# Optimization experiments

Measured on AMD Instinct MI355X. Metric: run time of the kernel, lower is better.

## Reference

```python
import jax, jax.numpy as jnp
import numpy as np
from jax import lax

N_LAYERS = 30
KERNEL = 5
MU = 255.0  # quantization_channels=256 -> mu = 255
DILATIONS = [(2 ** k) % 10 for k in range(N_LAYERS)]  # 2^k mod (n_layers/n_cycles)


def causal_conv1d(x, w, b, dilation):
    # x: [B,1,T], w: [1,1,K], b: [1]; left-pad so output is causal, same length.
    pad = (w.shape[-1] - 1) * dilation
    xp = jnp.pad(x, ((0, 0), (0, 0), (pad, 0)))
    y = lax.conv_general_dilated(xp, w, window_strides=(1,), padding='VALID',
                                 rhs_dilation=(dilation,),
                                 dimension_numbers=('NCH', 'OIH', 'NCH'))
    return y + b[None, :, None]


def setup_inputs() -> dict:
    key = jax.random.key(0)
    ks = jax.random.split(key, 12)
    B, T = 8, 262144
    s = 0.2  # keep gated activations away from saturation
    return {
        'x': jax.random.normal(ks[0], (B, 1, T), dtype=jnp.float32),
        'causal_w': jax.random.normal(ks[1], (1, 1, KERNEL), jnp.float32) * s,
        'causal_b': jnp.zeros((1,), jnp.float32),
        'filter_w': jax.random.normal(ks[2], (N_LAYERS, 1, 1, KERNEL), jnp.float32) * s,
        'filter_b': jax.random.normal(ks[3], (N_LAYERS, 1), jnp.float32) * s,
        'gate_w': jax.random.normal(ks[4], (N_LAYERS, 1, 1, KERNEL), jnp.float32) * s,
        'gate_b': jax.random.normal(ks[5], (N_LAYERS, 1), jnp.float32) * s,
        'res_w': jax.random.normal(ks[6], (N_LAYERS, 1, 1, 1), jnp.float32) * s,
        'res_b': jax.random.normal(ks[7], (N_LAYERS, 1), jnp.float32) * s,
        'conv1_w': jax.random.normal(ks[8], (1, 1, 1), jnp.float32) * s,
        'conv1_b': jnp.zeros((1,), jnp.float32),
        'conv2_w': jax.random.normal(ks[9], (1, 1, 1), jnp.float32) * s,
        'conv2_b': jnp.zeros((1,), jnp.float32),
    }


def reference(x, causal_w, causal_b, filter_w, filter_b, gate_w, gate_b,
              res_w, res_b, conv1_w, conv1_b, conv2_w, conv2_b):
    h = causal_conv1d(x, causal_w, causal_b, 1)
    skip_sum = jnp.zeros_like(h)
    for k in range(N_LAYERS):  # fixed small layer loop; dilation is static per layer
        d = DILATIONS[k]
        f = jnp.tanh(causal_conv1d(h, filter_w[k], filter_b[k], d))
        g = jax.nn.sigmoid(causal_conv1d(h, gate_w[k], gate_b[k], d))
        z = f * g
        skip_sum = skip_sum + z
        # 1x1 residual conv (1 channel) = scale + bias, then residual add
        h = z * res_w[k][0, 0, 0] + res_b[k][0] + h
    out = jax.nn.relu(skip_sum) * conv1_w[0, 0, 0] + conv1_b[0]
    out = jax.nn.relu(out) * conv2_w[0, 0, 0] + conv2_b[0]
    # mu-law expanding
    out = jnp.sign(out) * (jnp.power(1.0 + MU, jnp.abs(out)) - 1.0) / MU
    return jax.nn.softmax(out, axis=-1)
```

## Files before the change

### kernel.cpp

```cpp
#include <hip/hip_runtime.h>
#include <cmath>

#define T_LEN 262144
#define NROW 8
#define NL 30
#define NT 512
#define PPT 3
#define EXT (NT * PPT * 2)
#define HALO 576
#define TILE (EXT - HALO)
#define PB ((T_LEN + TILE - 1) / TILE)
#define PAD 32
#define CH 4096
#define RB (T_LEN / CH)
#define NB2 (NROW * RB)

#define NEG2LOG2E -2.885390082f
#define NEGLOG2E  -1.4426950409f

#if __has_builtin(__builtin_amdgcn_exp2f)
#define EXP2(x) __builtin_amdgcn_exp2f(x)
#else
#define EXP2(x) __expf(0.6931471805599453f * (x))
#endif

typedef float f32x2 __attribute__((ext_vector_type(2)));

__device__ __forceinline__ float fast_rcp(float x) { return __builtin_amdgcn_rcpf(x); }

__device__ __forceinline__ f32x2 exp2v(f32x2 x) {
    f32x2 r; r.x = EXP2(x.x); r.y = EXP2(x.y); return r;
}
__device__ __forceinline__ f32x2 rcpv(f32x2 x) {
    f32x2 r; r.x = fast_rcp(x.x); r.y = fast_rcp(x.y); return r;
}

template<int D, int CUT, bool WB>
__device__ __forceinline__ void layerv(
    int k,
    const float* __restrict__ fw, const float* __restrict__ fb,
    const float* __restrict__ gw, const float* __restrict__ gb,
    const float* __restrict__ rw, const float* __restrict__ rb,
    const float* __restrict__ src, float* __restrict__ dst,
    f32x2 (&h)[PPT], f32x2 (&skip)[PPT], int tid)
{
    const float f0 = fw[k*5+0], f1 = fw[k*5+1], f2 = fw[k*5+2], f3 = fw[k*5+3], f4 = fw[k*5+4];
    const float fbk = fb[k];
    const float g0 = gw[k*5+0], g1 = gw[k*5+1], g2 = gw[k*5+2], g3 = gw[k*5+3], g4 = gw[k*5+4];
    const float gbk = gb[k];
    const float rwk = rw[k], rbk = rb[k];

    #pragma unroll
    for (int p = 0; p < PPT; ++p) {
        const int i2 = 2 * (tid + p * NT);
        if (2 * p * NT < CUT) {
            if ((i2 + 1) < CUT) continue;
        }

        const f32x2 v0 = *(const f32x2*)&src[i2 - 4*D];
        const f32x2 v1 = *(const f32x2*)&src[i2 - 3*D];
        const f32x2 v2 = *(const f32x2*)&src[i2 - 2*D];
        const f32x2 v3 = *(const f32x2*)&src[i2 -   D];
        const f32x2 v4 = h[p];

        f32x2 af = fbk + f0 * v0;
        af = f1 * v1 + af;
        af = f2 * v2 + af;
        af = f3 * v3 + af;
        af = f4 * v4 + af;
        f32x2 ag = gbk + g0 * v0;
        ag = g1 * v1 + ag;
        ag = g2 * v2 + ag;
        ag = g3 * v3 + ag;
        ag = g4 * v4 + ag;

        const f32x2 u = exp2v(af * NEG2LOG2E);
        const f32x2 w = exp2v(ag * NEGLOG2E);
        const f32x2 num = 1.0f - u;
        const f32x2 den = (1.0f + u) * (1.0f + w);
        const f32x2 z = num * rcpv(den);
        skip[p] += z;
        if (WB) {
            h[p] = (z * rwk + rbk) + v4;
            *(f32x2*)&dst[i2] = h[p];
        }
    }
    if (WB) __syncthreads();
}

__device__ __forceinline__ void layer_d1(
    const float* __restrict__ fw, const float* __restrict__ fb,
    const float* __restrict__ gw, const float* __restrict__ gb,
    const float* __restrict__ rw, const float* __restrict__ rb,
    const float* __restrict__ src, float* __restrict__ dst,
    f32x2 (&h)[PPT], f32x2 (&skip)[PPT], int tid)
{
    const float f0 = fw[0], f1 = fw[1], f2 = fw[2], f3 = fw[3], f4 = fw[4];
    const float fbk = fb[0];
    const float g0 = gw[0], g1 = gw[1], g2 = gw[2], g3 = gw[3], g4 = gw[4];
    const float gbk = gb[0];
    const float rwk = rw[0], rbk = rb[0];

    #pragma unroll
    for (int p = 0; p < PPT; ++p) {
        const int i2 = 2 * (tid + p * NT);
        const f32x2 a = *(const f32x2*)&src[i2 - 4];
        const f32x2 b = *(const f32x2*)&src[i2 - 2];
        const f32x2 c = h[p];
        f32x2 v0, v1, v2, v3;
        v0.x = a.x; v0.y = a.y;
        v1.x = a.y; v1.y = b.x;
        v2.x = b.x; v2.y = b.y;
        v3.x = b.y; v3.y = c.x;

        f32x2 af = fbk + f0 * v0;
        af = f1 * v1 + af;
        af = f2 * v2 + af;
        af = f3 * v3 + af;
        af = f4 * c  + af;
        f32x2 ag = gbk + g0 * v0;
        ag = g1 * v1 + ag;
        ag = g2 * v2 + ag;
        ag = g3 * v3 + ag;
        ag = g4 * c  + ag;

        const f32x2 u = exp2v(af * NEG2LOG2E);
        const f32x2 w = exp2v(ag * NEGLOG2E);
        const f32x2 num = 1.0f - u;
        const f32x2 den = (1.0f + u) * (1.0f + w);
        const f32x2 z = num * rcpv(den);
        skip[p] += z;
        h[p] = (z * rwk + rbk) + c;
        *(f32x2*)&dst[i2] = h[p];
    }
    __syncthreads();
}

__global__ __launch_bounds__(NT, 8)
void k_wavenet(const float* __restrict__ x,
               const float* __restrict__ cw,  const float* __restrict__ cb,
               const float* __restrict__ fw,  const float* __restrict__ fb,
               const float* __restrict__ gw,  const float* __restrict__ gb,
               const float* __restrict__ rw,  const float* __restrict__ rb,
               const float* __restrict__ c1w, const float* __restrict__ c1b,
               const float* __restrict__ c2w, const float* __restrict__ c2b,
               float* __restrict__ eout, float* __restrict__ partsum)
{
    __shared__ __align__(16) float hrawA[PAD + EXT];
    __shared__ __align__(16) float hrawB[PAD + EXT];
    __shared__ float reds[NT / 64];
    float* bufA = hrawA + PAD;
    float* bufB = hrawB + PAD;

    const int tid  = threadIdx.x;
    const int row  = blockIdx.x / PB;
    const int tile = blockIdx.x % PB;
    const int t0   = tile * TILE;

    if (tid < PAD) { hrawA[tid] = 0.0f; hrawB[tid] = 0.0f; }

    const float* xr = x + (size_t)row * T_LEN;
    f32x2 h[PPT], skip[PPT];
    #pragma unroll
    for (int p = 0; p < PPT; ++p) {
        const int i2 = 2 * (tid + p * NT);
        const int g = t0 - HALO + i2;
        f32x2 v;
        v.x = (g     >= 0 && g     < T_LEN) ? xr[g]     : 0.0f;
        v.y = (g + 1 >= 0 && g + 1 < T_LEN) ? xr[g + 1] : 0.0f;
        *(f32x2*)&bufA[i2] = v;
        h[p] = v;
        skip[p].x = 0.0f; skip[p].y = 0.0f;
    }
    __syncthreads();

    {
        const float w0 = cw[0], w1 = cw[1], w2 = cw[2], w3 = cw[3], w4 = cw[4];
        const float b  = cb[0];
        #pragma unroll
        for (int p = 0; p < PPT; ++p) {
            const int i2 = 2 * (tid + p * NT);
            const f32x2 a  = *(const f32x2*)&bufA[i2 - 4];
            const f32x2 bb = *(const f32x2*)&bufA[i2 - 2];
            const f32x2 c  = h[p];
            f32x2 v0, v1, v2, v3;
            v0.x = a.x;  v0.y = a.y;
            v1.x = a.y;  v1.y = bb.x;
            v2.x = bb.x; v2.y = bb.y;
            v3.x = bb.y; v3.y = c.x;
            f32x2 acc = b + w0 * v0;
            acc = w1 * v1 + acc;
            acc = w2 * v2 + acc;
            acc = w3 * v3 + acc;
            acc = w4 * c  + acc;
            h[p] = acc;
            *(f32x2*)&bufB[i2] = acc;
        }
        __syncthreads();
    }

    layer_d1(fw, fb, gw, gb, rw, rb, bufB, bufA, h, skip, tid);
    layerv<2,  16, true >( 1, fw, fb, gw, gb, rw, rb, bufA, bufB, h, skip, tid);
    layerv<4,  32, true >( 2, fw, fb, gw, gb, rw, rb, bufB, bufA, h, skip, tid);
    layerv<8,  64, true >( 3, fw, fb, gw, gb, rw, rb, bufA, bufB, h, skip, tid);
    layerv<6,  88, true >( 4, fw, fb, gw, gb, rw, rb, bufB, bufA, h, skip, tid);
    layerv<2,  96, true >( 5, fw, fb, gw, gb, rw, rb, bufA, bufB, h, skip, tid);
    layerv<4, 112, true >( 6, fw, fb, gw, gb, rw, rb, bufB, bufA, h, skip, tid);
    layerv<8, 144, true >( 7, fw, fb, gw, gb, rw, rb, bufA, bufB, h, skip, tid);
    layerv<6, 168, true >( 8, fw, fb, gw, gb, rw, rb, bufB, bufA, h, skip, tid);
    layerv<2, 176, true >( 9, fw, fb, gw, gb, rw, rb, bufA, bufB, h, skip, tid);
    layerv<4, 192, true >(10, fw, fb, gw, gb, rw, rb, bufB, bufA, h, skip, tid);
    layerv<8, 224, true >(11, fw, fb, gw, gb, rw, rb, bufA, bufB, h, skip, tid);
    layerv<6, 248, true >(12, fw, fb, gw, gb, rw, rb, bufB, bufA, h, skip, tid);
    layerv<2, 256, true >(13, fw, fb, gw, gb, rw, rb, bufA, bufB, h, skip, tid);
    layerv<4, 272, true >(14, fw, fb, gw, gb, rw, rb, bufB, bufA, h, skip, tid);
    layerv<8, 304, true >(15, fw, fb, gw, gb, rw, rb, bufA, bufB, h, skip, tid);
    layerv<6, 328, true >(16, fw, fb, gw, gb, rw, rb, bufB, bufA, h, skip, tid);
    layerv<2, 336, true >(17, fw, fb, gw, gb, rw, rb, bufA, bufB, h, skip, tid);
    layerv<4, 352, true >(18, fw, fb, gw, gb, rw, rb, bufB, bufA, h, skip, tid);
    layerv<8, 384, true >(19, fw, fb, gw, gb, rw, rb, bufA, bufB, h, skip, tid);
    layerv<6, 408, true >(20, fw, fb, gw, gb, rw, rb, bufB, bufA, h, skip, tid);
    layerv<2, 416, true >(21, fw, fb, gw, gb, rw, rb, bufA, bufB, h, skip, tid);
    layerv<4, 432, true >(22, fw, fb, gw, gb, rw, rb, bufB, bufA, h, skip, tid);
    layerv<8, 464, true >(23, fw, fb, gw, gb, rw, rb, bufA, bufB, h, skip, tid);
    layerv<6, 488, true >(24, fw, fb, gw, gb, rw, rb, bufB, bufA, h, skip, tid);
    layerv<2, 496, true >(25, fw, fb, gw, gb, rw, rb, bufA, bufB, h, skip, tid);
    layerv<4, 512, true >(26, fw, fb, gw, gb, rw, rb, bufB, bufA, h, skip, tid);
    layerv<8, 544, true >(27, fw, fb, gw, gb, rw, rb, bufA, bufB, h, skip, tid);
    layerv<6, 568, true >(28, fw, fb, gw, gb, rw, rb, bufB, bufA, h, skip, tid);
    layerv<2, 576, false>(29, fw, fb, gw, gb, rw, rb, bufA, bufB, h, skip, tid);

    const float w1 = c1w[0], b1 = c1b[0], w2 = c2w[0], b2 = c2b[0];
    float s = 0.0f;
    float* er = eout + (size_t)row * T_LEN;
    #pragma unroll
    for (int p = 0; p < PPT; ++p) {
        const int i2 = 2 * (tid + p * NT);
        if (i2 >= HALO) {
            const int t = t0 + i2 - HALO;
            if (t < T_LEN) {
                f32x2 sk = skip[p];
                float ox = fmaf(fmaxf(sk.x, 0.0f), w1, b1);
                float oy = fmaf(fmaxf(sk.y, 0.0f), w1, b1);
                ox = fmaf(fmaxf(ox, 0.0f), w2, b2);
                oy = fmaf(fmaxf(oy, 0.0f), w2, b2);
                float vx = fmaf(EXP2(8.0f * fabsf(ox)), (1.0f/255.0f), -(1.0f/255.0f));
                float vy = fmaf(EXP2(8.0f * fabsf(oy)), (1.0f/255.0f), -(1.0f/255.0f));
                vx = copysignf(vx, ox);
                vy = copysignf(vy, oy);
                const float ex = __expf(vx);
                const float ey = __expf(vy);
                f32x2 e; e.x = ex; e.y = ey;
                *(f32x2*)&er[t] = e;
                s += ex + ey;
            }
        }
    }
    #pragma unroll
    for (int off = 32; off >= 1; off >>= 1) s += __shfl_xor(s, off, 64);
    if ((tid & 63) == 0) reds[tid >> 6] = s;
    __syncthreads();
    if (tid == 0) {
        float ss = 0.0f;
        #pragma unroll
        for (int w = 0; w < NT / 64; ++w) ss += reds[w];
        partsum[blockIdx.x] = ss;
    }
}

__global__ __launch_bounds__(256)
void k_scale(float* __restrict__ ebuf, const float* __restrict__ partsum)
{
    const int tid = threadIdx.x;
    const int row = blockIdx.x / RB;

    __shared__ float red[4];
    float s = 0.0f;
    for (int j = tid; j < PB; j += 256) s += partsum[row * PB + j];
    #pragma unroll
    for (int off = 32; off >= 1; off >>= 1) s += __shfl_xor(s, off, 64);
    if ((tid & 63) == 0) red[tid >> 6] = s;
    __syncthreads();
    const float tot = (red[0] + red[1]) + (red[2] + red[3]);
    const float inv = 1.0f / tot;

    float4* vp = (float4*)(ebuf + (size_t)blockIdx.x * CH);
    #pragma unroll
    for (int q = 0; q < 4; ++q) {
        float4 v = vp[tid + q * 256];
        v.x *= inv; v.y *= inv; v.z *= inv; v.w *= inv;
        vp[tid + q * 256] = v;
    }
}

extern "C" void kernel_launch(void* const* d_in, const int* in_sizes, int n_in,
                              void* d_out, int out_size, void* d_ws, size_t ws_size,
                              hipStream_t stream)
{
    const float* x   = (const float*)d_in[0];
    const float* cw  = (const float*)d_in[1];
    const float* cb  = (const float*)d_in[2];
    const float* fw  = (const float*)d_in[3];
    const float* fb  = (const float*)d_in[4];
    const float* gw  = (const float*)d_in[5];
    const float* gb  = (const float*)d_in[6];
    const float* rw  = (const float*)d_in[7];
    const float* rb  = (const float*)d_in[8];
    const float* c1w = (const float*)d_in[9];
    const float* c1b = (const float*)d_in[10];
    const float* c2w = (const float*)d_in[11];
    const float* c2b = (const float*)d_in[12];

    float* eout    = (float*)d_out;
    float* partsum = (float*)d_ws;

    k_wavenet<<<NROW * PB, NT, 0, stream>>>(x, cw, cb, fw, fb, gw, gb, rw, rb,
                                            c1w, c1b, c2w, c2b, eout, partsum);
    k_scale<<<NB2, 256, 0, stream>>>(eout, partsum);
}
```

Before: 144.3 us.

## Process two time tiles per block interleaved to share barriers and add ILP

Each block now carries two independent tiles through all 30 gated layers, with separate double-buffered LDS arrays for each. One __syncthreads per layer then serves both tiles, and the two independent dependency chains give the scheduler more instruction-level parallelism. This halves the grid, raises LDS per block and register pressure, and relaxes the launch-bounds occupancy hint. The softmax scale kernel is adjusted to read one partial sum per paired block and to use smaller chunks, which gives it more blocks.

```diff
diff --git a/kernel.cpp b/kernel.cpp
--- a/kernel.cpp
+++ b/kernel.cpp
@@ -9,9 +9,10 @@
 #define EXT (NT * PPT * 2)
 #define HALO 576
 #define TILE (EXT - HALO)
-#define PB ((T_LEN + TILE - 1) / TILE)
+#define PB 106
+#define JB (PB / 2)
 #define PAD 32
-#define CH 4096
+#define CH 2048
 #define RB (T_LEN / CH)
 #define NB2 (NROW * RB)
 
@@ -36,13 +37,15 @@
 }
 
 template<int D, int CUT, bool WB>
-__device__ __forceinline__ void layerv(
+__device__ __forceinline__ void layer2(
     int k,
     const float* __restrict__ fw, const float* __restrict__ fb,
     const float* __restrict__ gw, const float* __restrict__ gb,
     const float* __restrict__ rw, const float* __restrict__ rb,
-    const float* __restrict__ src, float* __restrict__ dst,
-    f32x2 (&h)[PPT], f32x2 (&skip)[PPT], int tid)
+    const float* __restrict__ s0, float* __restrict__ d0,
+    const float* __restrict__ s1, float* __restrict__ d1,
+    f32x2 (&h0)[PPT], f32x2 (&sk0)[PPT],
+    f32x2 (&h1)[PPT], f32x2 (&sk1)[PPT], int tid)
 {
     const float f0 = fw[k*5+0], f1 = fw[k*5+1], f2 = fw[k*5+2], f3 = fw[k*5+3], f4 = fw[k*5+4];
     const float fbk = fb[k];
@@ -50,50 +53,56 @@
     const float gbk = gb[k];
     const float rwk = rw[k], rbk = rb[k];
 
-    #pragma unroll
-    for (int p = 0; p < PPT; ++p) {
-        const int i2 = 2 * (tid + p * NT);
-        if (2 * p * NT < CUT) {
-            if ((i2 + 1) < CUT) continue;
+    auto body = [&](const float* __restrict__ src, float* __restrict__ dst,
+                    f32x2 (&h)[PPT], f32x2 (&skip)[PPT]) {
+        #pragma unroll
+        for (int p = 0; p < PPT; ++p) {
+            const int i2 = 2 * (tid + p * NT);
+            if (2 * p * NT < CUT) {
+                if ((i2 + 1) < CUT) continue;
+            }
+            const f32x2 v0 = *(const f32x2*)&src[i2 - 4*D];
+            const f32x2 v1 = *(const f32x2*)&src[i2 - 3*D];
+            const f32x2 v2 = *(const f32x2*)&src[i2 - 2*D];
+            const f32x2 v3 = *(const f32x2*)&src[i2 -   D];
+            const f32x2 v4 = h[p];
+
+            f32x2 af = fbk + f0 * v0;
+            af = f1 * v1 + af;
+            af = f2 * v2 + af;
+            af = f3 * v3 + af;
+            af = f4 * v4 + af;
+            f32x2 ag = gbk + g0 * v0;
+            ag = g1 * v1 + ag;
+            ag = g2 * v2 + ag;
+            ag = g3 * v3 + ag;
+            ag = g4 * v4 + ag;
+
+            const f32x2 u = exp2v(af * NEG2LOG2E);
+            const f32x2 w = exp2v(ag * NEGLOG2E);
+            const f32x2 num = 1.0f - u;
+            const f32x2 den = (1.0f + u) * (1.0f + w);
+            const f32x2 z = num * rcpv(den);
+            skip[p] += z;
+            if (WB) {
+                h[p] = (z * rwk + rbk) + v4;
+                *(f32x2*)&dst[i2] = h[p];
+            }
         }
-
-        const f32x2 v0 = *(const f32x2*)&src[i2 - 4*D];
-        const f32x2 v1 = *(const f32x2*)&src[i2 - 3*D];
-        const f32x2 v2 = *(const f32x2*)&src[i2 - 2*D];
-        const f32x2 v3 = *(const f32x2*)&src[i2 -   D];
-        const f32x2 v4 = h[p];
-
-        f32x2 af = fbk + f0 * v0;
-        af = f1 * v1 + af;
-        af = f2 * v2 + af;
-        af = f3 * v3 + af;
-        af = f4 * v4 + af;
-        f32x2 ag = gbk + g0 * v0;
-        ag = g1 * v1 + ag;
-        ag = g2 * v2 + ag;
-        ag = g3 * v3 + ag;
-        ag = g4 * v4 + ag;
-
-        const f32x2 u = exp2v(af * NEG2LOG2E);
-        const f32x2 w = exp2v(ag * NEGLOG2E);
-        const f32x2 num = 1.0f - u;
-        const f32x2 den = (1.0f + u) * (1.0f + w);
-        const f32x2 z = num * rcpv(den);
-        skip[p] += z;
-        if (WB) {
-            h[p] = (z * rwk + rbk) + v4;
-            *(f32x2*)&dst[i2] = h[p];
-        }
-    }
+    };
+    body(s0, d0, h0, sk0);
+    body(s1, d1, h1, sk1);
     if (WB) __syncthreads();
 }
 
-__device__ __forceinline__ void layer_d1(
+__device__ __forceinline__ void layer2_d1(
     const float* __restrict__ fw, const float* __restrict__ fb,
     const float* __restrict__ gw, const float* __restrict__ gb,
     const float* __restrict__ rw, const float* __restrict__ rb,
-    const float* __restrict__ src, float* __restrict__ dst,
-    f32x2 (&h)[PPT], f32x2 (&skip)[PPT], int tid)
+    const float* __restrict__ s0, float* __restrict__ d0,
+    const float* __restrict__ s1, float* __restrict__ d1,
+    f32x2 (&h0)[PPT], f32x2 (&sk0)[PPT],
+    f32x2 (&h1)[PPT], f32x2 (&sk1)[PPT], int tid)
 {
     const float f0 = fw[0], f1 = fw[1], f2 = fw[2], f3 = fw[3], f4 = fw[4];
     const float fbk = fb[0];
@@ -101,42 +110,47 @@
     const float gbk = gb[0];
     const float rwk = rw[0], rbk = rb[0];
 
-    #pragma unroll
-    for (int p = 0; p < PPT; ++p) {
-        const int i2 = 2 * (tid + p * NT);
-        const f32x2 a = *(const f32x2*)&src[i2 - 4];
-        const f32x2 b = *(const f32x2*)&src[i2 - 2];
-        const f32x2 c = h[p];
-        f32x2 v0, v1, v2, v3;
-        v0.x = a.x; v0.y = a.y;
-        v1.x = a.y; v1.y = b.x;
-        v2.x = b.x; v2.y = b.y;
-        v3.x = b.y; v3.y = c.x;
-
-        f32x2 af = fbk + f0 * v0;
-        af = f1 * v1 + af;
-        af = f2 * v2 + af;
-        af = f3 * v3 + af;
-        af = f4 * c  + af;
-        f32x2 ag = gbk + g0 * v0;
-        ag = g1 * v1 + ag;
-        ag = g2 * v2 + ag;
-        ag = g3 * v3 + ag;
-        ag = g4 * c  + ag;
-
-        const f32x2 u = exp2v(af * NEG2LOG2E);
-        const f32x2 w = exp2v(ag * NEGLOG2E);
-        const f32x2 num = 1.0f - u;
-        const f32x2 den = (1.0f + u) * (1.0f + w);
-        const f32x2 z = num * rcpv(den);
-        skip[p] += z;
-        h[p] = (z * rwk + rbk) + c;
-        *(f32x2*)&dst[i2] = h[p];
-    }
+    auto body = [&](const float* __restrict__ src, float* __restrict__ dst,
+                    f32x2 (&h)[PPT], f32x2 (&skip)[PPT]) {
+        #pragma unroll
+        for (int p = 0; p < PPT; ++p) {
+            const int i2 = 2 * (tid + p * NT);
+            const f32x2 a = *(const f32x2*)&src[i2 - 4];
+            const f32x2 b = *(const f32x2*)&src[i2 - 2];
+            const f32x2 c = h[p];
+            f32x2 v0, v1, v2, v3;
+            v0.x = a.x; v0.y = a.y;
+            v1.x = a.y; v1.y = b.x;
+            v2.x = b.x; v2.y = b.y;
+            v3.x = b.y; v3.y = c.x;
+
+            f32x2 af = fbk + f0 * v0;
+            af = f1 * v1 + af;
+            af = f2 * v2 + af;
+            af = f3 * v3 + af;
+            af = f4 * c  + af;
+            f32x2 ag = gbk + g0 * v0;
+            ag = g1 * v1 + ag;
+            ag = g2 * v2 + ag;
+            ag = g3 * v3 + ag;
+            ag = g4 * c  + ag;
+
+            const f32x2 u = exp2v(af * NEG2LOG2E);
+            const f32x2 w = exp2v(ag * NEGLOG2E);
+            const f32x2 num = 1.0f - u;
+            const f32x2 den = (1.0f + u) * (1.0f + w);
+            const f32x2 z = num * rcpv(den);
+            skip[p] += z;
+            h[p] = (z * rwk + rbk) + c;
+            *(f32x2*)&dst[i2] = h[p];
+        }
+    };
+    body(s0, d0, h0, sk0);
+    body(s1, d1, h1, sk1);
     __syncthreads();
 }
 
-__global__ __launch_bounds__(NT, 8)
+__global__ __launch_bounds__(NT, 4)
 void k_wavenet(const float* __restrict__ x,
                const float* __restrict__ cw,  const float* __restrict__ cb,
                const float* __restrict__ fw,  const float* __restrict__ fb,
@@ -146,116 +160,135 @@
                const float* __restrict__ c2w, const float* __restrict__ c2b,
                float* __restrict__ eout, float* __restrict__ partsum)
 {
-    __shared__ __align__(16) float hrawA[PAD + EXT];
-    __shared__ __align__(16) float hrawB[PAD + EXT];
+    __shared__ __align__(16) float rA0[PAD + EXT];
+    __shared__ __align__(16) float rB0[PAD + EXT];
+    __shared__ __align__(16) float rA1[PAD + EXT];
+    __shared__ __align__(16) float rB1[PAD + EXT];
     __shared__ float reds[NT / 64];
-    float* bufA = hrawA + PAD;
-    float* bufB = hrawB + PAD;
-
-    const int tid  = threadIdx.x;
-    const int row  = blockIdx.x / PB;
-    const int tile = blockIdx.x % PB;
-    const int t0   = tile * TILE;
-
-    if (tid < PAD) { hrawA[tid] = 0.0f; hrawB[tid] = 0.0f; }
+    float* A0 = rA0 + PAD;  float* B0 = rB0 + PAD;
+    float* A1 = rA1 + PAD;  float* B1 = rB1 + PAD;
+
+    const int tid = threadIdx.x;
+    const int row = blockIdx.x / JB;
+    const int jj  = blockIdx.x % JB;
+    const int t0a = (2 * jj)     * TILE;
+    const int t0b = (2 * jj + 1) * TILE;
+
+    if (tid < PAD) { rA0[tid] = 0.0f; rB0[tid] = 0.0f; rA1[tid] = 0.0f; rB1[tid] = 0.0f; }
 
     const float* xr = x + (size_t)row * T_LEN;
-    f32x2 h[PPT], skip[PPT];
-    #pragma unroll
-    for (int p = 0; p < PPT; ++p) {
-        const int i2 = 2 * (tid + p * NT);
-        const int g = t0 - HALO + i2;
-        f32x2 v;
-        v.x = (g     >= 0 && g     < T_LEN) ? xr[g]     : 0.0f;
-        v.y = (g + 1 >= 0 && g + 1 < T_LEN) ? xr[g + 1] : 0.0f;
-        *(f32x2*)&bufA[i2] = v;
-        h[p] = v;
-        skip[p].x = 0.0f; skip[p].y = 0.0f;
+    f32x2 h0[PPT], sk0[PPT], h1[PPT], sk1[PPT];
+
+    {
+        auto stage = [&](int t0, float* buf, f32x2 (&h)[PPT], f32x2 (&skip)[PPT]) {
+            #pragma unroll
+            for (int p = 0; p < PPT; ++p) {
+                const int i2 = 2 * (tid + p * NT);
+                const int g = t0 - HALO + i2;
+                f32x2 v;
+                v.x = (g     >= 0 && g     < T_LEN) ? xr[g]     : 0.0f;
+                v.y = (g + 1 >= 0 && g + 1 < T_LEN) ? xr[g + 1] : 0.0f;
+                *(f32x2*)&buf[i2] = v;
+                h[p] = v;
+                skip[p].x = 0.0f; skip[p].y = 0.0f;
+            }
+        };
+        stage(t0a, A0, h0, sk0);
+        stage(t0b, A1, h1, sk1);
+        __syncthreads();
     }
-    __syncthreads();
 
     {
         const float w0 = cw[0], w1 = cw[1], w2 = cw[2], w3 = cw[3], w4 = cw[4];
         const float b  = cb[0];
+        auto iconv = [&](const float* src, float* dst, f32x2 (&h)[PPT]) {
+            #pragma unroll
+            for (int p = 0; p < PPT; ++p) {
+                const int i2 = 2 * (tid + p * NT);
+                const f32x2 a  = *(const f32x2*)&src[i2 - 4];
+                const f32x2 bb = *(const f32x2*)&src[i2 - 2];
+                const f32x2 c  = h[p];
+                f32x2 v0, v1, v2, v3;
+                v0.x = a.x;  v0.y = a.y;
+                v1.x = a.y;  v1.y = bb.x;
+                v2.x = bb.x; v2.y = bb.y;
+                v3.x = bb.y; v3.y = c.x;
+                f32x2 acc = b + w0 * v0;
+                acc = w1 * v1 + acc;
+                acc = w2 * v2 + acc;
+                acc = w3 * v3 + acc;
+                acc = w4 * c  + acc;
+                h[p] = acc;
+                *(f32x2*)&dst[i2] = acc;
+            }
+        };
+        iconv(A0, B0, h0);
+        iconv(A1, B1, h1);
+        __syncthreads();
+    }
+
+    layer2_d1(fw, fb, gw, gb, rw, rb, B0, A0, B1, A1, h0, sk0, h1, sk1, tid);
+    layer2<2,  16, true >( 1, fw, fb, gw, gb, rw, rb, A0, B0, A1, B1, h0, sk0, h1, sk1, tid);
+    layer2<4,  32, true >( 2, fw, fb, gw, gb, rw, rb, B0, A0, B1, A1, h0, sk0, h1, sk1, tid);
+    layer2<8,  64, true >( 3, fw, fb, gw, gb, rw, rb, A0, B0, A1, B1, h0, sk0, h1, sk1, tid);
+    layer2<6,  88, true >( 4, fw, fb, gw, gb, rw, rb, B0, A0, B1, A1, h0, sk0, h1, sk1, tid);
+    layer2<2,  96, true >( 5, fw, fb, gw, gb, rw, rb, A0, B0, A1, B1, h0, sk0, h1, sk1, tid);
+    layer2<4, 112, true >( 6, fw, fb, gw, gb, rw, rb, B0, A0, B1, A1, h0, sk0, h1, sk1, tid);
+    layer2<8, 144, true >( 7, fw, fb, gw, gb, rw, rb, A0, B0, A1, B1, h0, sk0, h1, sk1, tid);
+    layer2<6, 168, true >( 8, fw, fb, gw, gb, rw, rb, B0, A0, B1, A1, h0, sk0, h1, sk1, tid);
+    layer2<2, 176, true >( 9, fw, fb, gw, gb, rw, rb, A0, B0, A1, B1, h0, sk0, h1, sk1, tid);
+    layer2<4, 192, true >(10, fw, fb, gw, gb, rw, rb, B0, A0, B1, A1, h0, sk0, h1, sk1, tid);
+    layer2<8, 224, true >(11, fw, fb, gw, gb, rw, rb, A0, B0, A1, B1, h0, sk0, h1, sk1, tid);
+    layer2<6, 248, true >(12, fw, fb, gw, gb, rw, rb, B0, A0, B1, A1, h0, sk0, h1, sk1, tid);
+    layer2<2, 256, true >(13, fw, fb, gw, gb, rw, rb, A0, B0, A1, B1, h0, sk0, h1, sk1, tid);
+    layer2<4, 272, true >(14, fw, fb, gw, gb, rw, rb, B0, A0, B1, A1, h0, sk0, h1, sk1, tid);
+    layer2<8, 304, true >(15, fw, fb, gw, gb, rw, rb, A0, B0, A1, B1, h0, sk0, h1, sk1, tid);
+    layer2<6, 328, true >(16, fw, fb, gw, gb, rw, rb, B0, A0, B1, A1, h0, sk0, h1, sk1, tid);
+    layer2<2, 336, true >(17, fw, fb, gw, gb, rw, rb, A0, B0, A1, B1, h0, sk0, h1, sk1, tid);
+    layer2<4, 352, true >(18, fw, fb, gw, gb, rw, rb, B0, A0, B1, A1, h0, sk0, h1, sk1, tid);
+    layer2<8, 384, true >(19, fw, fb, gw, gb, rw, rb, A0, B0, A1, B1, h0, sk0, h1, sk1, tid);
+    layer2<6, 408, true >(20, fw, fb, gw, gb, rw, rb, B0, A0, B1, A1, h0, sk0, h1, sk1, tid);
+    layer2<2, 416, true >(21, fw, fb, gw, gb, rw, rb, A0, B0, A1, B1, h0, sk0, h1, sk1, tid);
+    layer2<4, 432, true >(22, fw, fb, gw, gb, rw, rb, B0, A0, B1, A1, h0, sk0, h1, sk1, tid);
+    layer2<8, 464, true >(23, fw, fb, gw, gb, rw, rb, A0, B0, A1, B1, h0, sk0, h1, sk1, tid);
+    layer2<6, 488, true >(24, fw, fb, gw, gb, rw, rb, B0, A0, B1, A1, h0, sk0, h1, sk1, tid);
+    layer2<2, 496, true >(25, fw, fb, gw, gb, rw, rb, A0, B0, A1, B1, h0, sk0, h1, sk1, tid);
+    layer2<4, 512, true >(26, fw, fb, gw, gb, rw, rb, B0, A0, B1, A1, h0, sk0, h1, sk1, tid);
+    layer2<8, 544, true >(27, fw, fb, gw, gb, rw, rb, A0, B0, A1, B1, h0, sk0, h1, sk1, tid);
+    layer2<6, 568, true >(28, fw, fb, gw, gb, rw, rb, B0, A0, B1, A1, h0, sk0, h1, sk1, tid);
+    layer2<2, 576, false>(29, fw, fb, gw, gb, rw, rb, A0, B0, A1, B1, h0, sk0, h1, sk1, tid);
+
+    const float w1 = c1w[0], b1 = c1b[0], w2 = c2w[0], b2 = c2b[0];
+    float s = 0.0f;
+    float* er = eout + (size_t)row * T_LEN;
+    auto epi = [&](int t0, f32x2 (&skip)[PPT]) {
         #pragma unroll
         for (int p = 0; p < PPT; ++p) {
             const int i2 = 2 * (tid + p * NT);
-            const f32x2 a  = *(const f32x2*)&bufA[i2 - 4];
-            const f32x2 bb = *(const f32x2*)&bufA[i2 - 2];
-            const f32x2 c  = h[p];
-            f32x2 v0, v1, v2, v3;
-            v0.x = a.x;  v0.y = a.y;
-            v1.x = a.y;  v1.y = bb.x;
-            v2.x = bb.x; v2.y = bb.y;
-            v3.x = bb.y; v3.y = c.x;
-            f32x2 acc = b + w0 * v0;
-            acc = w1 * v1 + acc;
-            acc = w2 * v2 + acc;
-            acc = w3 * v3 + acc;
-            acc = w4 * c  + acc;
-            h[p] = acc;
-            *(f32x2*)&bufB[i2] = acc;
+            if (i2 >= HALO) {
+                const int t = t0 + i2 - HALO;
+                if (t < T_LEN) {
+                    f32x2 sk = skip[p];
+                    float ox = fmaf(fmaxf(sk.x, 0.0f), w1, b1);
+                    float oy = fmaf(fmaxf(sk.y, 0.0f), w1, b1);
+                    ox = fmaf(fmaxf(ox, 0.0f), w2, b2);
+                    oy = fmaf(fmaxf(oy, 0.0f), w2, b2);
+                    float vx = fmaf(EXP2(8.0f * fabsf(ox)), (1.0f/255.0f), -(1.0f/255.0f));
+                    float vy = fmaf(EXP2(8.0f * fabsf(oy)), (1.0f/255.0f), -(1.0f/255.0f));
+                    vx = copysignf(vx, ox);
+                    vy = copysignf(vy, oy);
+                    const float ex = __expf(vx);
+                    const float ey = __expf(vy);
+                    f32x2 e; e.x = ex; e.y = ey;
+                    *(f32x2*)&er[t] = e;
+                    s += ex + ey;
+                }
+            }
         }
-        __syncthreads();
-    }
-
-    layer_d1(fw, fb, gw, gb, rw, rb, bufB, bufA, h, skip, tid);
-    layerv<2,  16, true >( 1, fw, fb, gw, gb, rw, rb, bufA, bufB, h, skip, tid);
-    layerv<4,  32, true >( 2, fw, fb, gw, gb, rw, rb, bufB, bufA, h, skip, tid);
-    layerv<8,  64, true >( 3, fw, fb, gw, gb, rw, rb, bufA, bufB, h, skip, tid);
-    layerv<6,  88, true >( 4, fw, fb, gw, gb, rw, rb, bufB, bufA, h, skip, tid);
-    layerv<2,  96, true >( 5, fw, fb, gw, gb, rw, rb, bufA, bufB, h, skip, tid);
-    layerv<4, 112, true >( 6, fw, fb, gw, gb, rw, rb, bufB, bufA, h, skip, tid);
-    layerv<8, 144, true >( 7, fw, fb, gw, gb, rw, rb, bufA, bufB, h, skip, tid);
-    layerv<6, 168, true >( 8, fw, fb, gw, gb, rw, rb, bufB, bufA, h, skip, tid);
-    layerv<2, 176, true >( 9, fw, fb, gw, gb, rw, rb, bufA, bufB, h, skip, tid);
-    layerv<4, 192, true >(10, fw, fb, gw, gb, rw, rb, bufB, bufA, h, skip, tid);
-    layerv<8, 224, true >(11, fw, fb, gw, gb, rw, rb, bufA, bufB, h, skip, tid);
-    layerv<6, 248, true >(12, fw, fb, gw, gb, rw, rb, bufB, bufA, h, skip, tid);
-    layerv<2, 256, true >(13, fw, fb, gw, gb, rw, rb, bufA, bufB, h, skip, tid);
-    layerv<4, 272, true >(14, fw, fb, gw, gb, rw, rb, bufB, bufA, h, skip, tid);
-    layerv<8, 304, true >(15, fw, fb, gw, gb, rw, rb, bufA, bufB, h, skip, tid);
-    layerv<6, 328, true >(16, fw, fb, gw, gb, rw, rb, bufB, bufA, h, skip, tid);
-    layerv<2, 336, true >(17, fw, fb, gw, gb, rw, rb, bufA, bufB, h, skip, tid);
-    layerv<4, 352, true >(18, fw, fb, gw, gb, rw, rb, bufB, bufA, h, skip, tid);
-    layerv<8, 384, true >(19, fw, fb, gw, gb, rw, rb, bufA, bufB, h, skip, tid);
-    layerv<6, 408, true >(20, fw, fb, gw, gb, rw, rb, bufB, bufA, h, skip, tid);
-    layerv<2, 416, true >(21, fw, fb, gw, gb, rw, rb, bufA, bufB, h, skip, tid);
-    layerv<4, 432, true >(22, fw, fb, gw, gb, rw, rb, bufB, bufA, h, skip, tid);
-    layerv<8, 464, true >(23, fw, fb, gw, gb, rw, rb, bufA, bufB, h, skip, tid);
-    layerv<6, 488, true >(24, fw, fb, gw, gb, rw, rb, bufB, bufA, h, skip, tid);
-    layerv<2, 496, true >(25, fw, fb, gw, gb, rw, rb, bufA, bufB, h, skip, tid);
-    layerv<4, 512, true >(26, fw, fb, gw, gb, rw, rb, bufB, bufA, h, skip, tid);
-    layerv<8, 544, true >(27, fw, fb, gw, gb, rw, rb, bufA, bufB, h, skip, tid);
-    layerv<6, 568, true >(28, fw, fb, gw, gb, rw, rb, bufB, bufA, h, skip, tid);
-    layerv<2, 576, false>(29, fw, fb, gw, gb, rw, rb, bufA, bufB, h, skip, tid);
-
-    const float w1 = c1w[0], b1 = c1b[0], w2 = c2w[0], b2 = c2b[0];
-    float s = 0.0f;
-    float* er = eout + (size_t)row * T_LEN;
-    #pragma unroll
-    for (int p = 0; p < PPT; ++p) {
-        const int i2 = 2 * (tid + p * NT);
-        if (i2 >= HALO) {
-            const int t = t0 + i2 - HALO;
-            if (t < T_LEN) {
-                f32x2 sk = skip[p];
-                float ox = fmaf(fmaxf(sk.x, 0.0f), w1, b1);
-                float oy = fmaf(fmaxf(sk.y, 0.0f), w1, b1);
-                ox = fmaf(fmaxf(ox, 0.0f), w2, b2);
-                oy = fmaf(fmaxf(oy, 0.0f), w2, b2);
-                float vx = fmaf(EXP2(8.0f * fabsf(ox)), (1.0f/255.0f), -(1.0f/255.0f));
-                float vy = fmaf(EXP2(8.0f * fabsf(oy)), (1.0f/255.0f), -(1.0f/255.0f));
-                vx = copysignf(vx, ox);
-                vy = copysignf(vy, oy);
-                const float ex = __expf(vx);
-                const float ey = __expf(vy);
-                f32x2 e; e.x = ex; e.y = ey;
-                *(f32x2*)&er[t] = e;
-                s += ex + ey;
-            }
-        }
-    }
+    };
+    epi(t0a, sk0);
+    epi(t0b, sk1);
+
     #pragma unroll
     for (int off = 32; off >= 1; off >>= 1) s += __shfl_xor(s, off, 64);
     if ((tid & 63) == 0) reds[tid >> 6] = s;
@@ -275,8 +308,7 @@
     const int row = blockIdx.x / RB;
 
     __shared__ float red[4];
-    float s = 0.0f;
-    for (int j = tid; j < PB; j += 256) s += partsum[row * PB + j];
+    float s = (tid < JB) ? partsum[row * JB + tid] : 0.0f;
     #pragma unroll
     for (int off = 32; off >= 1; off >>= 1) s += __shfl_xor(s, off, 64);
     if ((tid & 63) == 0) red[tid >> 6] = s;
@@ -286,7 +318,7 @@
 
     float4* vp = (float4*)(ebuf + (size_t)blockIdx.x * CH);
     #pragma unroll
-    for (int q = 0; q < 4; ++q) {
+    for (int q = 0; q < 2; ++q) {
         float4 v = vp[tid + q * 256];
         v.x *= inv; v.y *= inv; v.z *= inv; v.w *= inv;
         vp[tid + q * 256] = v;
@@ -314,7 +346,7 @@
     float* eout    = (float*)d_out;
     float* partsum = (float*)d_ws;
 
-    k_wavenet<<<NROW * PB, NT, 0, stream>>>(x, cw, cb, fw, fb, gw, gb, rw, rb,
+    k_wavenet<<<NROW * JB, NT, 0, stream>>>(x, cw, cb, fw, fb, gw, gb, rw, rb,
                                             c1w, c1b, c2w, c2b, eout, partsum);
     k_scale<<<NB2, 256, 0, stream>>>(eout, partsum);
 }
```

New measurement: 152.8 us. 1.06x slower.

## Give each thread 8 contiguous samples and reuse dilated taps from registers

Applied to the files above, without the earlier changes.

Each thread now owns 8 consecutive time steps instead of 3 strided pairs, with 384 threads per block covering the same 3072-sample tile. Dilated-conv taps that fall inside the thread's own chunk come from registers, and only the halo before the chunk is read from shared memory with 16-byte loads. Global input loads, shared-memory write-backs and output stores are widened to float4. This cuts LDS traffic and instruction count per layer, at the cost of more registers per thread, a lower occupancy hint, and coarser per-thread skipping of halo work.

```diff
diff --git a/kernel.cpp b/kernel.cpp
--- a/kernel.cpp
+++ b/kernel.cpp
@@ -3,13 +3,11 @@
 
 #define T_LEN 262144
 #define NROW 8
-#define NL 30
-#define NT 512
-#define PPT 3
-#define EXT (NT * PPT * 2)
+#define NT 384
+#define EXT 3072
 #define HALO 576
 #define TILE (EXT - HALO)
-#define PB ((T_LEN + TILE - 1) / TILE)
+#define PB 106
 #define PAD 32
 #define CH 4096
 #define RB (T_LEN / CH)
@@ -25,6 +23,7 @@
 #endif
 
 typedef float f32x2 __attribute__((ext_vector_type(2)));
+typedef float f32x4 __attribute__((ext_vector_type(4)));
 
 __device__ __forceinline__ float fast_rcp(float x) { return __builtin_amdgcn_rcpf(x); }
 
@@ -34,15 +33,20 @@
 __device__ __forceinline__ f32x2 rcpv(f32x2 x) {
     f32x2 r; r.x = fast_rcp(x.x); r.y = fast_rcp(x.y); return r;
 }
+__device__ __forceinline__ f32x2 gatedv(f32x2 af, f32x2 ag) {
+    const f32x2 u = exp2v(af * NEG2LOG2E);
+    const f32x2 w = exp2v(ag * NEGLOG2E);
+    return (1.0f - u) * rcpv((1.0f + u) * (1.0f + w));
+}
 
 template<int D, int CUT, bool WB>
-__device__ __forceinline__ void layerv(
+__device__ __forceinline__ void layer8(
     int k,
     const float* __restrict__ fw, const float* __restrict__ fb,
     const float* __restrict__ gw, const float* __restrict__ gb,
     const float* __restrict__ rw, const float* __restrict__ rb,
     const float* __restrict__ src, float* __restrict__ dst,
-    f32x2 (&h)[PPT], f32x2 (&skip)[PPT], int tid)
+    f32x2 (&h)[4], f32x2 (&skip)[4], int base)
 {
     const float f0 = fw[k*5+0], f1 = fw[k*5+1], f2 = fw[k*5+2], f3 = fw[k*5+3], f4 = fw[k*5+4];
     const float fbk = fb[k];
@@ -50,17 +54,76 @@
     const float gbk = gb[k];
     const float rwk = rw[k], rbk = rb[k];
 
+    if (base >= CUT) {
+        f32x2 halo[2*D];
+        #pragma unroll
+        for (int j = 0; j < D; ++j) {
+            const f32x4 t4 = *(const f32x4*)&src[base - 4*D + 4*j];
+            f32x2 lo; lo.x = t4.x; lo.y = t4.y;
+            f32x2 hi; hi.x = t4.z; hi.y = t4.w;
+            halo[2*j]   = lo;
+            halo[2*j+1] = hi;
+        }
+        #pragma unroll
+        for (int p = 3; p >= 0; --p) {
+            const int r4 = p - 4*(D/2);
+            const int r3 = p - 3*(D/2);
+            const int r2 = p - 2*(D/2);
+            const int r1 = p - 1*(D/2);
+            const f32x2 v0 = (r4 >= 0) ? h[r4] : halo[2*D + r4];
+            const f32x2 v1 = (r3 >= 0) ? h[r3] : halo[2*D + r3];
+            const f32x2 v2 = (r2 >= 0) ? h[r2] : halo[2*D + r2];
+            const f32x2 v3 = (r1 >= 0) ? h[r1] : halo[2*D + r1];
+            const f32x2 v4 = h[p];
+
+            f32x2 af = fbk + f0 * v0;
+            af = f1 * v1 + af;
+            af = f2 * v2 + af;
+            af = f3 * v3 + af;
+            af = f4 * v4 + af;
+            f32x2 ag = gbk + g0 * v0;
+            ag = g1 * v1 + ag;
+            ag = g2 * v2 + ag;
+            ag = g3 * v3 + ag;
+            ag = g4 * v4 + ag;
+
+            const f32x2 z = gatedv(af, ag);
+            skip[p] += z;
+            if (WB) h[p] = (z * rwk + rbk) + v4;
+        }
+        if (WB) {
+            f32x4 lo; lo.x = h[0].x; lo.y = h[0].y; lo.z = h[1].x; lo.w = h[1].y;
+            f32x4 hi; hi.x = h[2].x; hi.y = h[2].y; hi.z = h[3].x; hi.w = h[3].y;
+            *(f32x4*)&dst[base]     = lo;
+            *(f32x4*)&dst[base + 4] = hi;
+        }
+    }
+    if (WB) __syncthreads();
+}
+
+__device__ __forceinline__ void layer8_d1(
+    const float* __restrict__ fw, const float* __restrict__ fb,
+    const float* __restrict__ gw, const float* __restrict__ gb,
+    const float* __restrict__ rw, const float* __restrict__ rb,
+    const float* __restrict__ src, float* __restrict__ dst,
+    f32x2 (&h)[4], f32x2 (&skip)[4], int base)
+{
+    const float f0 = fw[0], f1 = fw[1], f2 = fw[2], f3 = fw[3], f4 = fw[4];
+    const float fbk = fb[0];
+    const float g0 = gw[0], g1 = gw[1], g2 = gw[2], g3 = gw[3], g4 = gw[4];
+    const float gbk = gb[0];
+    const float rwk = rw[0], rbk = rb[0];
+
+    const f32x4 hl = *(const f32x4*)&src[base - 4];
+    const float w[12] = {hl.x, hl.y, hl.z, hl.w,
+                         h[0].x, h[0].y, h[1].x, h[1].y,
+                         h[2].x, h[2].y, h[3].x, h[3].y};
     #pragma unroll
-    for (int p = 0; p < PPT; ++p) {
-        const int i2 = 2 * (tid + p * NT);
-        if (2 * p * NT < CUT) {
-            if ((i2 + 1) < CUT) continue;
-        }
-
-        const f32x2 v0 = *(const f32x2*)&src[i2 - 4*D];
-        const f32x2 v1 = *(const f32x2*)&src[i2 - 3*D];
-        const f32x2 v2 = *(const f32x2*)&src[i2 - 2*D];
-        const f32x2 v3 = *(const f32x2*)&src[i2 -   D];
+    for (int p = 0; p < 4; ++p) {
+        f32x2 v0; v0.x = w[2*p+0]; v0.y = w[2*p+1];
+        f32x2 v1; v1.x = w[2*p+1]; v1.y = w[2*p+2];
+        f32x2 v2; v2.x = w[2*p+2]; v2.y = w[2*p+3];
+        f32x2 v3; v3.x = w[2*p+3]; v3.y = w[2*p+4];
         const f32x2 v4 = h[p];
 
         f32x2 af = fbk + f0 * v0;
@@ -74,69 +137,18 @@
         ag = g3 * v3 + ag;
         ag = g4 * v4 + ag;
 
-        const f32x2 u = exp2v(af * NEG2LOG2E);
-        const f32x2 w = exp2v(ag * NEGLOG2E);
-        const f32x2 num = 1.0f - u;
-        const f32x2 den = (1.0f + u) * (1.0f + w);
-        const f32x2 z = num * rcpv(den);
+        const f32x2 z = gatedv(af, ag);
         skip[p] += z;
-        if (WB) {
-            h[p] = (z * rwk + rbk) + v4;
-            *(f32x2*)&dst[i2] = h[p];
-        }
-    }
-    if (WB) __syncthreads();
-}
-
-__device__ __forceinline__ void layer_d1(
-    const float* __restrict__ fw, const float* __restrict__ fb,
-    const float* __restrict__ gw, const float* __restrict__ gb,
-    const float* __restrict__ rw, const float* __restrict__ rb,
-    const float* __restrict__ src, float* __restrict__ dst,
-    f32x2 (&h)[PPT], f32x2 (&skip)[PPT], int tid)
-{
-    const float f0 = fw[0], f1 = fw[1], f2 = fw[2], f3 = fw[3], f4 = fw[4];
-    const float fbk = fb[0];
-    const float g0 = gw[0], g1 = gw[1], g2 = gw[2], g3 = gw[3], g4 = gw[4];
-    const float gbk = gb[0];
-    const float rwk = rw[0], rbk = rb[0];
-
-    #pragma unroll
-    for (int p = 0; p < PPT; ++p) {
-        const int i2 = 2 * (tid + p * NT);
-        const f32x2 a = *(const f32x2*)&src[i2 - 4];
-        const f32x2 b = *(const f32x2*)&src[i2 - 2];
-        const f32x2 c = h[p];
-        f32x2 v0, v1, v2, v3;
-        v0.x = a.x; v0.y = a.y;
-        v1.x = a.y; v1.y = b.x;
-        v2.x = b.x; v2.y = b.y;
-        v3.x = b.y; v3.y = c.x;
-
-        f32x2 af = fbk + f0 * v0;
-        af = f1 * v1 + af;
-        af = f2 * v2 + af;
-        af = f3 * v3 + af;
-        af = f4 * c  + af;
-        f32x2 ag = gbk + g0 * v0;
-        ag = g1 * v1 + ag;
-        ag = g2 * v2 + ag;
-        ag = g3 * v3 + ag;
-        ag = g4 * c  + ag;
-
-        const f32x2 u = exp2v(af * NEG2LOG2E);
-        const f32x2 w = exp2v(ag * NEGLOG2E);
-        const f32x2 num = 1.0f - u;
-        const f32x2 den = (1.0f + u) * (1.0f + w);
-        const f32x2 z = num * rcpv(den);
-        skip[p] += z;
-        h[p] = (z * rwk + rbk) + c;
-        *(f32x2*)&dst[i2] = h[p];
-    }
+        h[p] = (z * rwk + rbk) + v4;
+    }
+    f32x4 lo; lo.x = h[0].x; lo.y = h[0].y; lo.z = h[1].x; lo.w = h[1].y;
+    f32x4 hi; hi.x = h[2].x; hi.y = h[2].y; hi.z = h[3].x; hi.w = h[3].y;
+    *(f32x4*)&dst[base]     = lo;
+    *(f32x4*)&dst[base + 4] = hi;
     __syncthreads();
 }
 
-__global__ __launch_bounds__(NT, 8)
+__global__ __launch_bounds__(NT, 4)
 void k_wavenet(const float* __restrict__ x,
                const float* __restrict__ cw,  const float* __restrict__ cb,
                const float* __restrict__ fw,  const float* __restrict__ fb,
@@ -146,99 +158,123 @@
                const float* __restrict__ c2w, const float* __restrict__ c2b,
                float* __restrict__ eout, float* __restrict__ partsum)
 {
-    __shared__ __align__(16) float hrawA[PAD + EXT];
-    __shared__ __align__(16) float hrawB[PAD + EXT];
+    __shared__ __align__(16) float rA[PAD + EXT];
+    __shared__ __align__(16) float rB[PAD + EXT];
     __shared__ float reds[NT / 64];
-    float* bufA = hrawA + PAD;
-    float* bufB = hrawB + PAD;
+    float* A = rA + PAD;
+    float* B = rB + PAD;
 
     const int tid  = threadIdx.x;
+    const int base = 8 * tid;
     const int row  = blockIdx.x / PB;
     const int tile = blockIdx.x % PB;
     const int t0   = tile * TILE;
 
-    if (tid < PAD) { hrawA[tid] = 0.0f; hrawB[tid] = 0.0f; }
+    if (tid < PAD / 4) {
+        f32x4 z4; z4.x = 0.f; z4.y = 0.f; z4.z = 0.f; z4.w = 0.f;
+        *(f32x4*)&rA[4*tid] = z4;
+        *(f32x4*)&rB[4*tid] = z4;
+    }
 
     const float* xr = x + (size_t)row * T_LEN;
-    f32x2 h[PPT], skip[PPT];
-    #pragma unroll
-    for (int p = 0; p < PPT; ++p) {
-        const int i2 = 2 * (tid + p * NT);
-        const int g = t0 - HALO + i2;
-        f32x2 v;
-        v.x = (g     >= 0 && g     < T_LEN) ? xr[g]     : 0.0f;
-        v.y = (g + 1 >= 0 && g + 1 < T_LEN) ? xr[g + 1] : 0.0f;
-        *(f32x2*)&bufA[i2] = v;
-        h[p] = v;
-        skip[p].x = 0.0f; skip[p].y = 0.0f;
+
+    if (t0 - HALO >= 0 && t0 - HALO + EXT <= T_LEN) {
+        #pragma unroll
+        for (int j = 0; j < 2; ++j) {
+            const int s = tid + j * NT;
+            *(f32x4*)&A[4*s] = *(const f32x4*)&xr[t0 - HALO + 4*s];
+        }
+    } else {
+        #pragma unroll
+        for (int j = 0; j < 2; ++j) {
+            const int s = tid + j * NT;
+            const int g = t0 - HALO + 4*s;
+            f32x4 v;
+            v.x = (g   >= 0 && g   < T_LEN) ? xr[g]   : 0.0f;
+            v.y = (g+1 >= 0 && g+1 < T_LEN) ? xr[g+1] : 0.0f;
+            v.z = (g+2 >= 0 && g+2 < T_LEN) ? xr[g+2] : 0.0f;
+            v.w = (g+3 >= 0 && g+3 < T_LEN) ? xr[g+3] : 0.0f;
+            *(f32x4*)&A[4*s] = v;
+        }
     }
     __syncthreads();
 
+    f32x2 h[4], skip[4];
     {
-        const float w0 = cw[0], w1 = cw[1], w2 = cw[2], w3 = cw[3], w4 = cw[4];
-        const float b  = cb[0];
-        #pragma unroll
-        for (int p = 0; p < PPT; ++p) {
-            const int i2 = 2 * (tid + p * NT);
-            const f32x2 a  = *(const f32x2*)&bufA[i2 - 4];
-            const f32x2 bb = *(const f32x2*)&bufA[i2 - 2];
-            const f32x2 c  = h[p];
-            f32x2 v0, v1, v2, v3;
-            v0.x = a.x;  v0.y = a.y;
-            v1.x = a.y;  v1.y = bb.x;
-            v2.x = bb.x; v2.y = bb.y;
-            v3.x = bb.y; v3.y = c.x;
-            f32x2 acc = b + w0 * v0;
-            acc = w1 * v1 + acc;
-            acc = w2 * v2 + acc;
-            acc = w3 * v3 + acc;
-            acc = w4 * c  + acc;
+        const f32x4 a = *(const f32x4*)&A[base];
+        const f32x4 b = *(const f32x4*)&A[base + 4];
+        h[0].x = a.x; h[0].y = a.y; h[1].x = a.z; h[1].y = a.w;
+        h[2].x = b.x; h[2].y = b.y; h[3].x = b.z; h[3].y = b.w;
+        #pragma unroll
+        for (int p = 0; p < 4; ++p) { skip[p].x = 0.f; skip[p].y = 0.f; }
+    }
+
+    {
+        const float q0 = cw[0], q1 = cw[1], q2 = cw[2], q3 = cw[3], q4 = cw[4];
+        const float qb = cb[0];
+        const f32x4 hl = *(const f32x4*)&A[base - 4];
+        const float w[12] = {hl.x, hl.y, hl.z, hl.w,
+                             h[0].x, h[0].y, h[1].x, h[1].y,
+                             h[2].x, h[2].y, h[3].x, h[3].y};
+        #pragma unroll
+        for (int p = 0; p < 4; ++p) {
+            f32x2 v0; v0.x = w[2*p+0]; v0.y = w[2*p+1];
+            f32x2 v1; v1.x = w[2*p+1]; v1.y = w[2*p+2];
+            f32x2 v2; v2.x = w[2*p+2]; v2.y = w[2*p+3];
+            f32x2 v3; v3.x = w[2*p+3]; v3.y = w[2*p+4];
+            f32x2 acc = qb + q0 * v0;
+            acc = q1 * v1 + acc;
+            acc = q2 * v2 + acc;
+            acc = q3 * v3 + acc;
+            acc = q4 * h[p] + acc;
             h[p] = acc;
-            *(f32x2*)&bufB[i2] = acc;
-        }
+        }
+        f32x4 lo; lo.x = h[0].x; lo.y = h[0].y; lo.z = h[1].x; lo.w = h[1].y;
+        f32x4 hi; hi.x = h[2].x; hi.y = h[2].y; hi.z = h[3].x; hi.w = h[3].y;
+        *(f32x4*)&B[base]     = lo;
+        *(f32x4*)&B[base + 4] = hi;
         __syncthreads();
     }
 
-    layer_d1(fw, fb, gw, gb, rw, rb, bufB, bufA, h, skip, tid);
-    layerv<2,  16, true >( 1, fw, fb, gw, gb, rw, rb, bufA, bufB, h, skip, tid);
-    layerv<4,  32, true >( 2, fw, fb, gw, gb, rw, rb, bufB, bufA, h, skip, tid);
-    layerv<8,  64, true >( 3, fw, fb, gw, gb, rw, rb, bufA, bufB, h, skip, tid);
-    layerv<6,  88, true >( 4, fw, fb, gw, gb, rw, rb, bufB, bufA, h, skip, tid);
-    layerv<2,  96, true >( 5, fw, fb, gw, gb, rw, rb, bufA, bufB, h, skip, tid);
-    layerv<4, 112, true >( 6, fw, fb, gw, gb, rw, rb, bufB, bufA, h, skip, tid);
-    layerv<8, 144, true >( 7, fw, fb, gw, gb, rw, rb, bufA, bufB, h, skip, tid);
-    layerv<6, 168, true >( 8, fw, fb, gw, gb, rw, rb, bufB, bufA, h, skip, tid);
-    layerv<2, 176, true >( 9, fw, fb, gw, gb, rw, rb, bufA, bufB, h, skip, tid);
-    layerv<4, 192, true >(10, fw, fb, gw, gb, rw, rb, bufB, bufA, h, skip, tid);
-    layerv<8, 224, true >(11, fw, fb, gw, gb, rw, rb, bufA, bufB, h, skip, tid);
-    layerv<6, 248, true >(12, fw, fb, gw, gb, rw, rb, bufB, bufA, h, skip, tid);
-    layerv<2, 256, true >(13, fw, fb, gw, gb, rw, rb, bufA, bufB, h, skip, tid);
-    layerv<4, 272, true >(14, fw, fb, gw, gb, rw, rb, bufB, bufA, h, skip, tid);
-    layerv<8, 304, true >(15, fw, fb, gw, gb, rw, rb, bufA, bufB, h, skip, tid);
-    layerv<6, 328, true >(16, fw, fb, gw, gb, rw, rb, bufB, bufA, h, skip, tid);
-    layerv<2, 336, true >(17, fw, fb, gw, gb, rw, rb, bufA, bufB, h, skip, tid);
-    layerv<4, 352, true >(18, fw, fb, gw, gb, rw, rb, bufB, bufA, h, skip, tid);
-    layerv<8, 384, true >(19, fw, fb, gw, gb, rw, rb, bufA, bufB, h, skip, tid);
-    layerv<6, 408, true >(20, fw, fb, gw, gb, rw, rb, bufB, bufA, h, skip, tid);
-    layerv<2, 416, true >(21, fw, fb, gw, gb, rw, rb, bufA, bufB, h, skip, tid);
-    layerv<4, 432, true >(22, fw, fb, gw, gb, rw, rb, bufB, bufA, h, skip, tid);
-    layerv<8, 464, true >(23, fw, fb, gw, gb, rw, rb, bufA, bufB, h, skip, tid);
-    layerv<6, 488, true >(24, fw, fb, gw, gb, rw, rb, bufB, bufA, h, skip, tid);
-    layerv<2, 496, true >(25, fw, fb, gw, gb, rw, rb, bufA, bufB, h, skip, tid);
-    layerv<4, 512, true >(26, fw, fb, gw, gb, rw, rb, bufB, bufA, h, skip, tid);
-    layerv<8, 544, true >(27, fw, fb, gw, gb, rw, rb, bufA, bufB, h, skip, tid);
-    layerv<6, 568, true >(28, fw, fb, gw, gb, rw, rb, bufB, bufA, h, skip, tid);
-    layerv<2, 576, false>(29, fw, fb, gw, gb, rw, rb, bufA, bufB, h, skip, tid);
+    layer8_d1(fw, fb, gw, gb, rw, rb, B, A, h, skip, base);
+    layer8<2,  16, true >( 1, fw, fb, gw, gb, rw, rb, A, B, h, skip, base);
+    layer8<4,  32, true >( 2, fw, fb, gw, gb, rw, rb, B, A, h, skip, base);
+    layer8<8,  64, true >( 3, fw, fb, gw, gb, rw, rb, A, B, h, skip, base);
+    layer8<6,  88, true >( 4, fw, fb, gw, gb, rw, rb, B, A, h, skip, base);
+    layer8<2,  96, true >( 5, fw, fb, gw, gb, rw, rb, A, B, h, skip, base);
+    layer8<4, 112, true >( 6, fw, fb, gw, gb, rw, rb, B, A, h, skip, base);
+    layer8<8, 144, true >( 7, fw, fb, gw, gb, rw, rb, A, B, h, skip, base);
+    layer8<6, 168, true >( 8, fw, fb, gw, gb, rw, rb, B, A, h, skip, base);
+    layer8<2, 176, true >( 9, fw, fb, gw, gb, rw, rb, A, B, h, skip, base);
+    layer8<4, 192, true >(10, fw, fb, gw, gb, rw, rb, B, A, h, skip, base);
+    layer8<8, 224, true >(11, fw, fb, gw, gb, rw, rb, A, B, h, skip, base);
+    layer8<6, 248, true >(12, fw, fb, gw, gb, rw, rb, B, A, h, skip, base);
+    layer8<2, 256, true >(13, fw, fb, gw, gb, rw, rb, A, B, h, skip, base);
+    layer8<4, 272, true >(14, fw, fb, gw, gb, rw, rb, B, A, h, skip, base);
+    layer8<8, 304, true >(15, fw, fb, gw, gb, rw, rb, A, B, h, skip, base);
+    layer8<6, 328, true >(16, fw, fb, gw, gb, rw, rb, B, A, h, skip, base);
+    layer8<2, 336, true >(17, fw, fb, gw, gb, rw, rb, A, B, h, skip, base);
+    layer8<4, 352, true >(18, fw, fb, gw, gb, rw, rb, B, A, h, skip, base);
+    layer8<8, 384, true >(19, fw, fb, gw, gb, rw, rb, A, B, h, skip, base);
+    layer8<6, 408, true >(20, fw, fb, gw, gb, rw, rb, B, A, h, skip, base);
+    layer8<2, 416, true >(21, fw, fb, gw, gb, rw, rb, A, B, h, skip, base);
+    layer8<4, 432, true >(22, fw, fb, gw, gb, rw, rb, B, A, h, skip, base);
+    layer8<8, 464, true >(23, fw, fb, gw, gb, rw, rb, A, B, h, skip, base);
+    layer8<6, 488, true >(24, fw, fb, gw, gb, rw, rb, B, A, h, skip, base);
+    layer8<2, 496, true >(25, fw, fb, gw, gb, rw, rb, A, B, h, skip, base);
+    layer8<4, 512, true >(26, fw, fb, gw, gb, rw, rb, B, A, h, skip, base);
+    layer8<8, 544, true >(27, fw, fb, gw, gb, rw, rb, A, B, h, skip, base);
+    layer8<6, 568, true >(28, fw, fb, gw, gb, rw, rb, B, A, h, skip, base);
+    layer8<2, 576, false>(29, fw, fb, gw, gb, rw, rb, A, B, h, skip, base);
 
     const float w1 = c1w[0], b1 = c1b[0], w2 = c2w[0], b2 = c2b[0];
     float s = 0.0f;
-    float* er = eout + (size_t)row * T_LEN;
-    #pragma unroll
-    for (int p = 0; p < PPT; ++p) {
-        const int i2 = 2 * (tid + p * NT);
-        if (i2 >= HALO) {
-            const int t = t0 + i2 - HALO;
-            if (t < T_LEN) {
+    if (base >= HALO) {
+        const int t = t0 + base - HALO;
+        if (t < T_LEN) {
+            float e8[8];
+            #pragma unroll
+            for (int p = 0; p < 4; ++p) {
                 f32x2 sk = skip[p];
                 float ox = fmaf(fmaxf(sk.x, 0.0f), w1, b1);
                 float oy = fmaf(fmaxf(sk.y, 0.0f), w1, b1);
@@ -250,10 +286,14 @@
                 vy = copysignf(vy, oy);
                 const float ex = __expf(vx);
                 const float ey = __expf(vy);
-                f32x2 e; e.x = ex; e.y = ey;
-                *(f32x2*)&er[t] = e;
+                e8[2*p] = ex; e8[2*p+1] = ey;
                 s += ex + ey;
             }
+            float* er = eout + (size_t)row * T_LEN + t;
+            f32x4 lo; lo.x = e8[0]; lo.y = e8[1]; lo.z = e8[2]; lo.w = e8[3];
+            f32x4 hi; hi.x = e8[4]; hi.y = e8[5]; hi.z = e8[6]; hi.w = e8[7];
+            *(f32x4*)&er[0] = lo;
+            *(f32x4*)&er[4] = hi;
         }
     }
     #pragma unroll
```

Measured after the change: 153.0 us. +6.0%, slower.
